# Kernel optimization log

Hardware: AMD Instinct MI355X
Metric: run time of the kernel (lower is better)

## Reference

```python
import jax, jax.numpy as jnp
import numpy as np

LOG2 = 0.6931471805599453
CUTOFF = 5.0
NG = 25

def ssp(x):
    # shifted softplus used throughout schnetpack
    return jax.nn.softplus(x) - LOG2

def setup_inputs() -> dict:
    key = jax.random.key(0)
    ks = jax.random.split(key, 10)
    B, A, N, F, Z, L = 8, 1024, 64, 128, 100, 3
    atomic_numbers = jax.random.randint(ks[0], (B, A), 0, Z, dtype=jnp.int32)
    positions = jax.random.normal(ks[1], (B, A, 3), dtype=jnp.float32) * 3.0
    cell = jnp.zeros((B, 3, 3), jnp.float32)
    cell_offset = jnp.zeros((B, A, N, 3), jnp.float32)
    neighbors = jax.random.randint(ks[2], (B, A, N), 0, A, dtype=jnp.int32)
    neighbor_mask = jnp.ones((B, A, N), jnp.float32)
    embed = (jax.random.normal(ks[3], (Z, F), dtype=jnp.float32) * 0.1).at[0].set(0.0)  # padding_idx=0
    p = lambda k, s: jax.random.normal(k, s, dtype=jnp.float32) * 0.1
    return dict(
        atomic_numbers=atomic_numbers, positions=positions, cell=cell,
        cell_offset=cell_offset, neighbors=neighbors, neighbor_mask=neighbor_mask,
        embed=embed,
        fw1=p(ks[4], (L, NG, F)), fb1=jnp.zeros((L, F), jnp.float32),
        fw2=p(ks[5], (L, F, F)), fb2=jnp.zeros((L, F), jnp.float32),
        in2f_w=p(ks[6], (L, F, F)),
        f2out_w=p(ks[7], (L, F, F)), f2out_b=jnp.zeros((L, F), jnp.float32),
        dense_w=p(ks[8], (L, F, F)), dense_b=jnp.zeros((L, F), jnp.float32),
    )

def reference(atomic_numbers, positions, cell, cell_offset, neighbors, neighbor_mask,
              embed, fw1, fb1, fw2, fb2, in2f_w, f2out_w, f2out_b, dense_w, dense_b):
    gather = jax.vmap(lambda a, i: a[i])  # per-batch neighbor gather
    x = embed[atomic_numbers]                                   # (B,A,F)
    # AtomDistances
    pos_j = gather(positions, neighbors)                        # (B,A,N,3)
    off = jnp.einsum('bani,bij->banj', cell_offset, cell)
    vec = pos_j - positions[:, :, None, :] + off
    d2 = jnp.sum(vec * vec, axis=-1)                            # (B,A,N)
    mask = neighbor_mask
    r = jnp.sqrt(jnp.where(mask > 0, d2, 1.0)) * mask           # masked distances
    # GaussianSmearing(0, cutoff, NG)
    goff = jnp.linspace(0.0, CUTOFF, NG)
    width = goff[1] - goff[0]
    f_ij = jnp.exp((-0.5 / (width * width)) * (r[..., None] - goff) ** 2)  # (B,A,N,NG)
    # CosineCutoff
    C = 0.5 * (jnp.cos(r * jnp.pi / CUTOFF) + 1.0) * (r < CUTOFF)
    for l in range(fw1.shape[0]):
        # filter-generating network (Dense+ssp, Dense)
        W = ssp(f_ij @ fw1[l] + fb1[l]) @ fw2[l] + fb2[l]       # (B,A,N,F)
        W = W * C[..., None]
        # CFConv: in2f (no bias) -> gather -> multiply -> masked sum -> f2out(ssp)
        y = x @ in2f_w[l]                                       # (B,A,F)
        y = gather(y, neighbors) * W * mask[..., None]          # (B,A,N,F)
        agg = jnp.sum(y, axis=2)                                # (B,A,F)
        v = ssp(agg @ f2out_w[l] + f2out_b[l])
        v = v @ dense_w[l] + dense_b[l]                         # interaction output dense
        x = x + v
    return x
```

## Files before the change

kernel.cpp:

```cpp
#include <hip/hip_runtime.h>
#include <hip/hip_fp16.h>
#include <math.h>

#define BB 8
#define AA 1024
#define NN 64
#define FF 128
#define NG 25

#define WIDTH 0.2083333333f
#define COEF  (-0.5f/(WIDTH*WIDTH))
#define PI_F  3.14159265358979f
#define CUTOFF 5.0f

#define KT 2048
#define HT (CUTOFF/(KT-1))
#define INVH ((float)(KT-1)/CUTOFF)

#define STR 132

typedef __attribute__((ext_vector_type(8))) short bf16x8;
typedef __attribute__((ext_vector_type(4))) short bf16x4;
typedef __attribute__((ext_vector_type(4))) float f32x4;

__device__ __forceinline__ float sspf(float x){
    return fmaxf(x, 0.f) + log1pf(expf(-fabsf(x))) - 0.69314718056f;
}
__device__ __forceinline__ short bf16r(float x){
    union { float f; unsigned u; } v; v.f = x;
    unsigned r = v.u + 0x7FFF + ((v.u >> 16) & 1);
    return (short)(r >> 16);
}
__device__ __forceinline__ __half2 h2bc(unsigned u){
    union { unsigned u; __half2 h; } v; v.u = u; return v.h;
}

__global__ __launch_bounds__(512) void k_prep(const float* __restrict__ pos,
                        const float* __restrict__ cell,
                        const float* __restrict__ coff, const int* __restrict__ nbr,
                        const float* __restrict__ mask,
                        const int* __restrict__ z, const float* __restrict__ emb,
                        const float* __restrict__ fw1, const float* __restrict__ fb1,
                        const float* __restrict__ fw2, const float* __restrict__ fb2,
                        const float* __restrict__ in2f, const float* __restrict__ f2w,
                        const float* __restrict__ dw,
                        unsigned* __restrict__ codes, int* __restrict__ cnt,
                        short* __restrict__ Wp,
                        __half* __restrict__ T, float* __restrict__ x,
                        __half* __restrict__ y){
    __shared__ __align__(16) char smem[NG*FF*4 + 16*28*4 + 16*STR*2];
    float* s_w1 = (float*)smem;
    float* s_g  = (float*)(smem + NG*FF*4);
    short* s_a  = (short*)(smem + NG*FF*4 + 16*28*4);
    __shared__ int s_cnt[16];

    int p = blockIdx.x;
    int tid = threadIdx.x, wv = tid >> 6, lane = tid & 63;
    int m = lane & 15, q = lane >> 4;
    int col = 16*wv + m;

    if(p < 512){
        int row0 = ((p & 7)*64 + (p >> 3))*16;
        if(tid < 16) s_cnt[tid] = 0;
        __syncthreads();
        #pragma unroll
        for(int u = 0; u < 2; u++){
            int pr = 2*tid + u;
            int rr = pr >> 6, n = pr & 63;
            int row = row0 + rr;
            int b = row >> 10;
            int flat = row*NN + n;
            int j = nbr[flat];
            const float* pi = pos + (size_t)row*3;
            const float* pj = pos + (size_t)(b*AA + j)*3;
            const float* co = coff + (size_t)flat*3;
            const float* cl = cell + b*9;
            float ox = co[0]*cl[0] + co[1]*cl[3] + co[2]*cl[6];
            float oy = co[0]*cl[1] + co[1]*cl[4] + co[2]*cl[7];
            float oz = co[0]*cl[2] + co[1]*cl[5] + co[2]*cl[8];
            float vx = pj[0]-pi[0]+ox, vy = pj[1]-pi[1]+oy, vz = pj[2]-pi[2]+oz;
            float d2 = vx*vx + vy*vy + vz*vz;
            float mk = mask[flat];
            float r  = sqrtf(mk > 0.f ? d2 : 1.0f) * mk;
            if(mk > 0.f && r < CUTOFF){
                int iv = (int)(r*INVH + 0.5f);
                if(iv > KT-1) iv = KT-1;
                int pos_ = atomicAdd(&s_cnt[rr], 1);
                codes[row*NN + pos_] = (unsigned)iv | ((unsigned)j << 16);
            }
        }
        __syncthreads();
        if(tid < 16){
            int c = s_cnt[tid];
            cnt[row0 + tid] = c;
            int cp = (c + 3) & ~3;
            for(int k2 = c; k2 < cp; k2++)
                codes[(row0 + tid)*NN + k2] = (unsigned)(KT-1);
        }
        bf16x8 wf[4];
        #pragma unroll
        for(int ks = 0; ks < 4; ks++)
            #pragma unroll
            for(int i = 0; i < 8; i++)
                wf[ks][i] = bf16r(in2f[(32*ks + 8*q + i)*FF + col]);
        for(int i = tid; i < 16*FF; i += 512){
            int rr = i >> 7, f = i & (FF-1);
            float v = emb[z[row0+rr]*FF + f];
            x[(row0+rr)*FF + f] = v;
            s_a[rr*STR + f] = bf16r(v);
        }
        __syncthreads();
        f32x4 acc = {0.f,0.f,0.f,0.f};
        #pragma unroll
        for(int ks = 0; ks < 4; ks++){
            const short* ap = s_a + m*STR + 32*ks + 8*q;
            bf16x4 lo = *(const bf16x4*)ap;
            bf16x4 hi = *(const bf16x4*)(ap + 4);
            bf16x8 af;
            af[0]=lo[0]; af[1]=lo[1]; af[2]=lo[2]; af[3]=lo[3];
            af[4]=hi[0]; af[5]=hi[1]; af[6]=hi[2]; af[7]=hi[3];
            acc = __builtin_amdgcn_mfma_f32_16x16x32_bf16(af, wf[ks], acc, 0, 0, 0);
        }
        #pragma unroll
        for(int j = 0; j < 4; j++)
            y[(row0 + 4*q + j)*FF + col] = __float2half(acc[j]);
    } else if(p < 896){
        int tb = p - 512;
        int l = tb >> 7;
        int kb = tb & 127;
        const float* w2s = fw2 + l*16384;
        bf16x8 wf[4];
        #pragma unroll
        for(int ks = 0; ks < 4; ks++)
            #pragma unroll
            for(int i = 0; i < 8; i++)
                wf[ks][i] = bf16r(w2s[(32*ks + 8*q + i)*FF + col]);

        for(int i = tid; i < NG*FF; i += 512) s_w1[i] = fw1[l*NG*FF + i];
        for(int i = tid; i < 16*NG; i += 512){
            int kn = i/25, g = i - 25*kn;
            float d = (16*kb + kn)*HT - g*WIDTH;
            s_g[kn*28 + g] = expf(COEF*d*d);
        }
        __syncthreads();
        {
            int f = tid & (FF-1), g4 = tid >> 7;
            float b1v = fb1[l*FF + f];
            #pragma unroll
            for(int i = 0; i < 4; i++){
                int kn = g4 + 4*i;
                float zz = b1v;
                for(int g = 0; g < NG; g++)
                    zz = fmaf(s_g[kn*28 + g], s_w1[g*FF + f], zz);
                s_a[kn*STR + f] = bf16r(sspf(zz));
            }
        }
        __syncthreads();
        float b2 = fb2[l*FF + col];
        f32x4 acc = {b2, b2, b2, b2};
        #pragma unroll
        for(int ks = 0; ks < 4; ks++){
            const short* ap = s_a + m*STR + 32*ks + 8*q;
            bf16x4 lo = *(const bf16x4*)ap;
            bf16x4 hi = *(const bf16x4*)(ap + 4);
            bf16x8 af;
            af[0]=lo[0]; af[1]=lo[1]; af[2]=lo[2]; af[3]=lo[3];
            af[4]=hi[0]; af[5]=hi[1]; af[6]=hi[2]; af[7]=hi[3];
            acc = __builtin_amdgcn_mfma_f32_16x16x32_bf16(af, wf[ks], acc, 0, 0, 0);
        }
        #pragma unroll
        for(int j = 0; j < 4; j++){
            int kn = 16*kb + 4*q + j;
            float r = kn*HT;
            float C = (r < CUTOFF) ? 0.5f*(cosf(r*(PI_F/CUTOFF)) + 1.0f) : 0.f;
            T[(l*KT + kn)*FF + col] = __float2half(acc[j]*C);
        }
    } else {
        int idx = (p - 896)*512 + tid;
        int id = idx >> 14, rem = idx & 16383;
        int ks = rem >> 12, nt = (rem >> 9) & 7, ln = (rem >> 3) & 63, i = rem & 7;
        int k = 32*ks + 8*(ln >> 4) + i;
        int f = 16*nt + (ln & 15);
        const float* src = (id < 3) ? f2w + id*16384
                         : (id < 6) ? dw  + (id-3)*16384
                                    : in2f + (id-5)*16384;
        Wp[idx] = bf16r(src[k*FF + f]);
    }
}

__global__ __launch_bounds__(512) void k_layerM(const unsigned* __restrict__ codes,
                                                const int* __restrict__ cnt,
                                                const __half* __restrict__ Tl,
                                                const __half* __restrict__ yin,
                                                const short* __restrict__ w1p,
                                                const float* __restrict__ f2b,
                                                const short* __restrict__ w2p,
                                                const float* __restrict__ db,
                                                const short* __restrict__ w3p,
                                                float* __restrict__ x,
                                                __half* __restrict__ ynext){
    __shared__ unsigned s_code[16*NN];
    __shared__ short s_a[16*STR];
    __shared__ short s_t[16*STR];

    int tid = threadIdx.x, wv = tid >> 6, lane = tid & 63;
    int m = lane & 15, q = lane >> 4;
    int p = blockIdx.x;
    int b = p & 7;
    int row0 = (b*64 + (p >> 3))*16;
    int col = 16*wv + m;

    float bias1 = f2b[col], bias2 = db[col];
    float xr[4];
    #pragma unroll
    for(int j = 0; j < 4; j++) xr[j] = x[(row0 + 4*q + j)*FF + col];

    *(uint2*)&s_code[2*tid] = *(const uint2*)&codes[row0*NN + 2*tid];
    __syncthreads();

    int qf = lane >> 4, fl = lane & 15, f8 = 8*fl;
    const __half* yb = yin + ((size_t)b*AA << 7) + f8;
    const __half* tb = Tl + f8;
    int a0 = 2*wv, a1 = 2*wv + 1;
    int n0 = (cnt[row0 + a0] + 3) >> 2;
    int n1 = (cnt[row0 + a1] + 3) >> 2;
    int nmax = n0 > n1 ? n0 : n1;
    __half2 hz = __float2half2_rn(0.f);
    __half2 pa[4] = {hz,hz,hz,hz}, pb[4] = {hz,hz,hz,hz};
    float ca[8] = {0,0,0,0,0,0,0,0}, cb[8] = {0,0,0,0,0,0,0,0};
    #pragma unroll 2
    for(int t = 0; t < nmax; t++){
        if(t < n0){
            unsigned cda = s_code[a0*NN + 4*t + qf];
            uint4 tva = *(const uint4*)(tb + ((cda & 0xFFFFu) << 7));
            uint4 yva = *(const uint4*)(yb + ((size_t)(cda >> 16) << 7));
            pa[0] = __hfma2(h2bc(tva.x), h2bc(yva.x), pa[0]);
            pa[1] = __hfma2(h2bc(tva.y), h2bc(yva.y), pa[1]);
            pa[2] = __hfma2(h2bc(tva.z), h2bc(yva.z), pa[2]);
            pa[3] = __hfma2(h2bc(tva.w), h2bc(yva.w), pa[3]);
        }
        if(t < n1){
            unsigned cdb = s_code[a1*NN + 4*t + qf];
            uint4 tvb = *(const uint4*)(tb + ((cdb & 0xFFFFu) << 7));
            uint4 yvb = *(const uint4*)(yb + ((size_t)(cdb >> 16) << 7));
            pb[0] = __hfma2(h2bc(tvb.x), h2bc(yvb.x), pb[0]);
            pb[1] = __hfma2(h2bc(tvb.y), h2bc(yvb.y), pb[1]);
            pb[2] = __hfma2(h2bc(tvb.z), h2bc(yvb.z), pb[2]);
            pb[3] = __hfma2(h2bc(tvb.w), h2bc(yvb.w), pb[3]);
        }
        if((t & 3) == 3){
            #pragma unroll
            for(int c2 = 0; c2 < 4; c2++){
                float2 ua = __half22float2(pa[c2]);
                float2 ub = __half22float2(pb[c2]);
                ca[2*c2]   += ua.x; ca[2*c2+1] += ua.y;
                cb[2*c2]   += ub.x; cb[2*c2+1] += ub.y;
                pa[c2] = hz; pb[c2] = hz;
            }
        }
    }
    #pragma unroll
    for(int c2 = 0; c2 < 4; c2++){
        float2 ua = __half22float2(pa[c2]);
        float2 ub = __half22float2(pb[c2]);
        ca[2*c2]   += ua.x; ca[2*c2+1] += ua.y;
        cb[2*c2]   += ub.x; cb[2*c2+1] += ub.y;
    }
    #pragma unroll
    for(int i = 0; i < 8; i++){
        ca[i] += __shfl_xor(ca[i], 16);
        ca[i] += __shfl_xor(ca[i], 32);
        cb[i] += __shfl_xor(cb[i], 16);
        cb[i] += __shfl_xor(cb[i], 32);
    }
    if(qf == 0){
        unsigned w0 = (unsigned short)bf16r(ca[0]) | ((unsigned)(unsigned short)bf16r(ca[1]) << 16);
        unsigned w1 = (unsigned short)bf16r(ca[2]) | ((unsigned)(unsigned short)bf16r(ca[3]) << 16);
        unsigned w2 = (unsigned short)bf16r(ca[4]) | ((unsigned)(unsigned short)bf16r(ca[5]) << 16);
        unsigned w3 = (unsigned short)bf16r(ca[6]) | ((unsigned)(unsigned short)bf16r(ca[7]) << 16);
        uint2 u01 = {w0, w1}, u23 = {w2, w3};
        *(uint2*)&s_a[a0*STR + f8]     = u01;
        *(uint2*)&s_a[a0*STR + f8 + 4] = u23;
        unsigned v0 = (unsigned short)bf16r(cb[0]) | ((unsigned)(unsigned short)bf16r(cb[1]) << 16);
        unsigned v1 = (unsigned short)bf16r(cb[2]) | ((unsigned)(unsigned short)bf16r(cb[3]) << 16);
        unsigned v2 = (unsigned short)bf16r(cb[4]) | ((unsigned)(unsigned short)bf16r(cb[5]) << 16);
        unsigned v3 = (unsigned short)bf16r(cb[6]) | ((unsigned)(unsigned short)bf16r(cb[7]) << 16);
        uint2 s01 = {v0, v1}, s23 = {v2, v3};
        *(uint2*)&s_a[a1*STR + f8]     = s01;
        *(uint2*)&s_a[a1*STR + f8 + 4] = s23;
    }

    unsigned long long w1o = (unsigned long long)w1p;
    asm volatile("" : "+s"(w1o));
    bf16x8 wfa[4];
    {
        const bf16x8* w1v = (const bf16x8*)w1o;
        #pragma unroll
        for(int ks = 0; ks < 4; ks++) wfa[ks] = w1v[(ks*8 + wv)*64 + lane];
    }
    __syncthreads();

    f32x4 acc = {bias1, bias1, bias1, bias1};
    #pragma unroll
    for(int ks = 0; ks < 4; ks++){
        const short* ap = s_a + m*STR + 32*ks + 8*q;
        bf16x4 lo = *(const bf16x4*)ap;
        bf16x4 hi = *(const bf16x4*)(ap + 4);
        bf16x8 af;
        af[0]=lo[0]; af[1]=lo[1]; af[2]=lo[2]; af[3]=lo[3];
        af[4]=hi[0]; af[5]=hi[1]; af[6]=hi[2]; af[7]=hi[3];
        acc = __builtin_amdgcn_mfma_f32_16x16x32_bf16(af, wfa[ks], acc, 0, 0, 0);
    }

    unsigned long long w2o = (unsigned long long)w2p;
    asm volatile("" : "+s"(w2o));
    bf16x8 wfb[4];
    {
        const bf16x8* w2v = (const bf16x8*)w2o;
        #pragma unroll
        for(int ks = 0; ks < 4; ks++) wfb[ks] = w2v[(ks*8 + wv)*64 + lane];
    }

    #pragma unroll
    for(int j = 0; j < 4; j++)
        s_t[(4*q + j)*STR + col] = bf16r(sspf(acc[j]));
    __syncthreads();

    f32x4 a2 = {bias2, bias2, bias2, bias2};
    #pragma unroll
    for(int ks = 0; ks < 4; ks++){
        const short* ap = s_t + m*STR + 32*ks + 8*q;
        bf16x4 lo = *(const bf16x4*)ap;
        bf16x4 hi = *(const bf16x4*)(ap + 4);
        bf16x8 af;
        af[0]=lo[0]; af[1]=lo[1]; af[2]=lo[2]; af[3]=lo[3];
        af[4]=hi[0]; af[5]=hi[1]; af[6]=hi[2]; af[7]=hi[3];
        a2 = __builtin_amdgcn_mfma_f32_16x16x32_bf16(af, wfb[ks], a2, 0, 0, 0);
    }

    float xn[4];
    #pragma unroll
    for(int j = 0; j < 4; j++){
        xn[j] = xr[j] + a2[j];
        x[(row0 + 4*q + j)*FF + col] = xn[j];
    }
    if(w3p){
        unsigned long long w3o = (unsigned long long)w3p;
        asm volatile("" : "+s"(w3o));
        bf16x8 wfc[4];
        {
            const bf16x8* w3v = (const bf16x8*)w3o;
            #pragma unroll
            for(int ks = 0; ks < 4; ks++) wfc[ks] = w3v[(ks*8 + wv)*64 + lane];
        }
        #pragma unroll
        for(int j = 0; j < 4; j++)
            s_a[(4*q + j)*STR + col] = bf16r(xn[j]);
        __syncthreads();
        f32x4 a3 = {0.f, 0.f, 0.f, 0.f};
        #pragma unroll
        for(int ks = 0; ks < 4; ks++){
            const short* ap = s_a + m*STR + 32*ks + 8*q;
            bf16x4 lo = *(const bf16x4*)ap;
            bf16x4 hi = *(const bf16x4*)(ap + 4);
            bf16x8 af;
            af[0]=lo[0]; af[1]=lo[1]; af[2]=lo[2]; af[3]=lo[3];
            af[4]=hi[0]; af[5]=hi[1]; af[6]=hi[2]; af[7]=hi[3];
            a3 = __builtin_amdgcn_mfma_f32_16x16x32_bf16(af, wfc[ks], a3, 0, 0, 0);
        }
        #pragma unroll
        for(int j = 0; j < 4; j++)
            ynext[(row0 + 4*q + j)*FF + col] = __float2half(a3[j]);
    }
}

extern "C" void kernel_launch(void* const* d_in, const int* in_sizes, int n_in,
                              void* d_out, int out_size, void* d_ws, size_t ws_size,
                              hipStream_t stream) {
    const int*   zat  = (const int*)  d_in[0];
    const float* pos  = (const float*)d_in[1];
    const float* cell = (const float*)d_in[2];
    const float* coff = (const float*)d_in[3];
    const int*   nbr  = (const int*)  d_in[4];
    const float* mask = (const float*)d_in[5];
    const float* emb  = (const float*)d_in[6];
    const float* fw1  = (const float*)d_in[7];
    const float* fb1  = (const float*)d_in[8];
    const float* fw2  = (const float*)d_in[9];
    const float* fb2  = (const float*)d_in[10];
    const float* in2f = (const float*)d_in[11];
    const float* f2w  = (const float*)d_in[12];
    const float* f2b  = (const float*)d_in[13];
    const float* dw   = (const float*)d_in[14];
    const float* db   = (const float*)d_in[15];

    float* x = (float*)d_out;
    unsigned* codes = (unsigned*)d_ws;
    __half* Tb = (__half*)(codes + BB*AA*NN);
    __half* yA = Tb + 3*KT*FF;
    __half* yB = yA + BB*AA*FF;
    short*  Wp = (short*)(yB + BB*AA*FF);
    int*    cnt = (int*)(Wp + 8*16384);

    k_prep<<<1152, 512, 0, stream>>>(pos, cell, coff, nbr, mask, zat, emb,
                                     fw1, fb1, fw2, fb2, in2f, f2w, dw,
                                     codes, cnt, Wp, Tb, x, yA);

    k_layerM<<<BB*AA/16, 512, 0, stream>>>(codes, cnt, Tb,           yA,
                                           Wp + 0*16384, f2b,        Wp + 3*16384, db,
                                           Wp + 6*16384, x, yB);
    k_layerM<<<BB*AA/16, 512, 0, stream>>>(codes, cnt, Tb + KT*FF,   yB,
                                           Wp + 1*16384, f2b + FF,   Wp + 4*16384, db + FF,
                                           Wp + 7*16384, x, yA);
    k_layerM<<<BB*AA/16, 512, 0, stream>>>(codes, cnt, Tb + 2*KT*FF, yA,
                                           Wp + 2*16384, f2b + 2*FF, Wp + 5*16384, db + 2*FF,
                                           nullptr, x, nullptr);
}
```

Before: 59.17 us.

## Fuse prep and three layer kernels into one cooperative persistent kernel

Replaces the four kernel launches (prep plus three layer kernels) with a single cooperative kernel of 512 blocks that uses grid-wide syncs between phases. Each block keeps its neighbor codes in shared memory and its x rows in registers across layers, so the global codes, counts and x round trips go away. Launch gaps are removed in exchange for grid barriers, and the whole grid must be co-resident, which depends on the occupancy check. If that check or the cooperative launch fails, the old multi-kernel path runs instead.

```diff
diff --git a/kernel.cpp b/kernel.cpp
--- a/kernel.cpp
+++ b/kernel.cpp
@@ -1,6 +1,9 @@
 #include <hip/hip_runtime.h>
 #include <hip/hip_fp16.h>
+#include <hip/hip_cooperative_groups.h>
 #include <math.h>
+
+namespace cg = cooperative_groups;
 
 #define BB 8
 #define AA 1024
@@ -33,6 +36,333 @@
 }
 __device__ __forceinline__ __half2 h2bc(unsigned u){
     union { unsigned u; __half2 h; } v; v.u = u; return v.h;
+}
+
+__global__ __launch_bounds__(512, 4) void k_all(const float* __restrict__ pos,
+                        const float* __restrict__ cell,
+                        const float* __restrict__ coff, const int* __restrict__ nbr,
+                        const float* __restrict__ mask,
+                        const int* __restrict__ z, const float* __restrict__ emb,
+                        const float* __restrict__ fw1, const float* __restrict__ fb1,
+                        const float* __restrict__ fw2, const float* __restrict__ fb2,
+                        const float* __restrict__ in2f, const float* __restrict__ f2w,
+                        const float* __restrict__ f2b, const float* __restrict__ dw,
+                        const float* __restrict__ db,
+                        short* __restrict__ Wp, __half* __restrict__ T,
+                        float* __restrict__ x, __half* __restrict__ yA,
+                        __half* __restrict__ yB){
+    __shared__ unsigned s_code[16*NN];
+    __shared__ int s_cnt[16];
+    __shared__ __align__(16) char smem[NG*FF*4 + 16*28*4 + 16*STR*2];
+
+    int p = blockIdx.x;
+    int tid = threadIdx.x, wv = tid >> 6, lane = tid & 63;
+    int m = lane & 15, q = lane >> 4;
+    int col = 16*wv + m;
+    int row0 = ((p & 7)*64 + (p >> 3))*16;
+    int b = row0 >> 10;
+
+    float* s_w1 = (float*)smem;
+    float* s_g  = (float*)(smem + NG*FF*4);
+    short* s_pa = (short*)(smem + NG*FF*4 + 16*28*4);
+
+    if(tid < 16) s_cnt[tid] = 0;
+    __syncthreads();
+    #pragma unroll
+    for(int u = 0; u < 2; u++){
+        int pr = 2*tid + u;
+        int rr = pr >> 6, n = pr & 63;
+        int row = row0 + rr;
+        int flat = row*NN + n;
+        int j = nbr[flat];
+        const float* pi = pos + (size_t)row*3;
+        const float* pj = pos + (size_t)(b*AA + j)*3;
+        const float* co = coff + (size_t)flat*3;
+        const float* cl = cell + b*9;
+        float ox = co[0]*cl[0] + co[1]*cl[3] + co[2]*cl[6];
+        float oy = co[0]*cl[1] + co[1]*cl[4] + co[2]*cl[7];
+        float oz = co[0]*cl[2] + co[1]*cl[5] + co[2]*cl[8];
+        float vx = pj[0]-pi[0]+ox, vy = pj[1]-pi[1]+oy, vz = pj[2]-pi[2]+oz;
+        float d2 = vx*vx + vy*vy + vz*vz;
+        float mk = mask[flat];
+        float r  = sqrtf(mk > 0.f ? d2 : 1.0f) * mk;
+        if(mk > 0.f && r < CUTOFF){
+            int iv = (int)(r*INVH + 0.5f);
+            if(iv > KT-1) iv = KT-1;
+            int ps = atomicAdd(&s_cnt[rr], 1);
+            s_code[rr*NN + ps] = (unsigned)iv | ((unsigned)j << 16);
+        }
+    }
+    __syncthreads();
+    if(tid < 16){
+        int c = s_cnt[tid];
+        int cp = (c + 3) & ~3;
+        for(int k2 = c; k2 < cp; k2++)
+            s_code[tid*NN + k2] = (unsigned)(KT-1);
+    }
+
+    float xr[4];
+    #pragma unroll
+    for(int j = 0; j < 4; j++) xr[j] = emb[z[row0 + 4*q + j]*FF + col];
+    for(int i = tid; i < 16*FF; i += 512){
+        int rr = i >> 7, f = i & (FF-1);
+        s_pa[rr*STR + f] = bf16r(emb[z[row0+rr]*FF + f]);
+    }
+    bf16x8 wf0[4];
+    #pragma unroll
+    for(int ks = 0; ks < 4; ks++)
+        #pragma unroll
+        for(int i = 0; i < 8; i++)
+            wf0[ks][i] = bf16r(in2f[(32*ks + 8*q + i)*FF + col]);
+    __syncthreads();
+    {
+        f32x4 acc = {0.f,0.f,0.f,0.f};
+        #pragma unroll
+        for(int ks = 0; ks < 4; ks++){
+            const short* ap = s_pa + m*STR + 32*ks + 8*q;
+            bf16x4 lo = *(const bf16x4*)ap;
+            bf16x4 hi = *(const bf16x4*)(ap + 4);
+            bf16x8 af;
+            af[0]=lo[0]; af[1]=lo[1]; af[2]=lo[2]; af[3]=lo[3];
+            af[4]=hi[0]; af[5]=hi[1]; af[6]=hi[2]; af[7]=hi[3];
+            acc = __builtin_amdgcn_mfma_f32_16x16x32_bf16(af, wf0[ks], acc, 0, 0, 0);
+        }
+        #pragma unroll
+        for(int j = 0; j < 4; j++)
+            yA[(row0 + 4*q + j)*FF + col] = __float2half(acc[j]);
+    }
+
+    if(p < 384){
+        __syncthreads();
+        int l = p >> 7, kb = p & 127;
+        const float* w2s = fw2 + l*16384;
+        bf16x8 wf[4];
+        #pragma unroll
+        for(int ks = 0; ks < 4; ks++)
+            #pragma unroll
+            for(int i = 0; i < 8; i++)
+                wf[ks][i] = bf16r(w2s[(32*ks + 8*q + i)*FF + col]);
+        for(int i = tid; i < NG*FF; i += 512) s_w1[i] = fw1[l*NG*FF + i];
+        for(int i = tid; i < 16*NG; i += 512){
+            int kn = i/25, g = i - 25*kn;
+            float d = (16*kb + kn)*HT - g*WIDTH;
+            s_g[kn*28 + g] = expf(COEF*d*d);
+        }
+        __syncthreads();
+        {
+            int f = tid & (FF-1), g4 = tid >> 7;
+            float b1v = fb1[l*FF + f];
+            #pragma unroll
+            for(int i = 0; i < 4; i++){
+                int kn = g4 + 4*i;
+                float zz = b1v;
+                for(int g = 0; g < NG; g++)
+                    zz = fmaf(s_g[kn*28 + g], s_w1[g*FF + f], zz);
+                s_pa[kn*STR + f] = bf16r(sspf(zz));
+            }
+        }
+        __syncthreads();
+        float b2 = fb2[l*FF + col];
+        f32x4 acc = {b2, b2, b2, b2};
+        #pragma unroll
+        for(int ks = 0; ks < 4; ks++){
+            const short* ap = s_pa + m*STR + 32*ks + 8*q;
+            bf16x4 lo = *(const bf16x4*)ap;
+            bf16x4 hi = *(const bf16x4*)(ap + 4);
+            bf16x8 af;
+            af[0]=lo[0]; af[1]=lo[1]; af[2]=lo[2]; af[3]=lo[3];
+            af[4]=hi[0]; af[5]=hi[1]; af[6]=hi[2]; af[7]=hi[3];
+            acc = __builtin_amdgcn_mfma_f32_16x16x32_bf16(af, wf[ks], acc, 0, 0, 0);
+        }
+        #pragma unroll
+        for(int j = 0; j < 4; j++){
+            int kn = 16*kb + 4*q + j;
+            float r = kn*HT;
+            float C = (r < CUTOFF) ? 0.5f*(cosf(r*(PI_F/CUTOFF)) + 1.0f) : 0.f;
+            T[(l*KT + kn)*FF + col] = __float2half(acc[j]*C);
+        }
+    } else {
+        int base = (p - 384)*1024;
+        #pragma unroll
+        for(int e = 0; e < 2; e++){
+            int idx = base + e*512 + tid;
+            int id = idx >> 14, rem = idx & 16383;
+            int ks = rem >> 12, nt = (rem >> 9) & 7, ln = (rem >> 3) & 63, i = rem & 7;
+            int k = 32*ks + 8*(ln >> 4) + i;
+            int f = 16*nt + (ln & 15);
+            const float* src = (id < 3) ? f2w + id*16384
+                             : (id < 6) ? dw  + (id-3)*16384
+                                        : in2f + (id-5)*16384;
+            Wp[idx] = bf16r(src[k*FF + f]);
+        }
+    }
+
+    cg::this_grid().sync();
+
+    short* s_a = (short*)smem;
+    short* s_t = (short*)(smem + 16*STR*2);
+    int qf = lane >> 4, fl = lane & 15, f8 = 8*fl;
+    int a0 = 2*wv, a1 = 2*wv + 1;
+    int n0 = (s_cnt[a0] + 3) >> 2;
+    int n1 = (s_cnt[a1] + 3) >> 2;
+    int nmax = n0 > n1 ? n0 : n1;
+
+    for(int l = 0; l < 3; l++){
+        const __half* yin  = (l == 1) ? yB : yA;
+        __half*       yout = (l == 0) ? yB : yA;
+        const __half* tb = T + (size_t)l*KT*FF + f8;
+        const __half* yb = yin + ((size_t)b*AA << 7) + f8;
+        float bias1 = f2b[l*FF + col], bias2 = db[l*FF + col];
+
+        __half2 hz = __float2half2_rn(0.f);
+        __half2 pa[4] = {hz,hz,hz,hz}, pb[4] = {hz,hz,hz,hz};
+        float ca[8] = {0,0,0,0,0,0,0,0}, cb[8] = {0,0,0,0,0,0,0,0};
+        #pragma unroll 2
+        for(int t = 0; t < nmax; t++){
+            if(t < n0){
+                unsigned cda = s_code[a0*NN + 4*t + qf];
+                uint4 tva = *(const uint4*)(tb + ((cda & 0xFFFFu) << 7));
+                uint4 yva = *(const uint4*)(yb + ((size_t)(cda >> 16) << 7));
+                pa[0] = __hfma2(h2bc(tva.x), h2bc(yva.x), pa[0]);
+                pa[1] = __hfma2(h2bc(tva.y), h2bc(yva.y), pa[1]);
+                pa[2] = __hfma2(h2bc(tva.z), h2bc(yva.z), pa[2]);
+                pa[3] = __hfma2(h2bc(tva.w), h2bc(yva.w), pa[3]);
+            }
+            if(t < n1){
+                unsigned cdb = s_code[a1*NN + 4*t + qf];
+                uint4 tvb = *(const uint4*)(tb + ((cdb & 0xFFFFu) << 7));
+                uint4 yvb = *(const uint4*)(yb + ((size_t)(cdb >> 16) << 7));
+                pb[0] = __hfma2(h2bc(tvb.x), h2bc(yvb.x), pb[0]);
+                pb[1] = __hfma2(h2bc(tvb.y), h2bc(yvb.y), pb[1]);
+                pb[2] = __hfma2(h2bc(tvb.z), h2bc(yvb.z), pb[2]);
+                pb[3] = __hfma2(h2bc(tvb.w), h2bc(yvb.w), pb[3]);
+            }
+            if((t & 3) == 3){
+                #pragma unroll
+                for(int c2 = 0; c2 < 4; c2++){
+                    float2 ua = __half22float2(pa[c2]);
+                    float2 ub = __half22float2(pb[c2]);
+                    ca[2*c2]   += ua.x; ca[2*c2+1] += ua.y;
+                    cb[2*c2]   += ub.x; cb[2*c2+1] += ub.y;
+                    pa[c2] = hz; pb[c2] = hz;
+                }
+            }
+        }
+        #pragma unroll
+        for(int c2 = 0; c2 < 4; c2++){
+            float2 ua = __half22float2(pa[c2]);
+            float2 ub = __half22float2(pb[c2]);
+            ca[2*c2]   += ua.x; ca[2*c2+1] += ua.y;
+            cb[2*c2]   += ub.x; cb[2*c2+1] += ub.y;
+        }
+        #pragma unroll
+        for(int i = 0; i < 8; i++){
+            ca[i] += __shfl_xor(ca[i], 16);
+            ca[i] += __shfl_xor(ca[i], 32);
+            cb[i] += __shfl_xor(cb[i], 16);
+            cb[i] += __shfl_xor(cb[i], 32);
+        }
+        if(qf == 0){
+            unsigned w0 = (unsigned short)bf16r(ca[0]) | ((unsigned)(unsigned short)bf16r(ca[1]) << 16);
+            unsigned w1 = (unsigned short)bf16r(ca[2]) | ((unsigned)(unsigned short)bf16r(ca[3]) << 16);
+            unsigned w2 = (unsigned short)bf16r(ca[4]) | ((unsigned)(unsigned short)bf16r(ca[5]) << 16);
+            unsigned w3 = (unsigned short)bf16r(ca[6]) | ((unsigned)(unsigned short)bf16r(ca[7]) << 16);
+            uint2 u01 = {w0, w1}, u23 = {w2, w3};
+            *(uint2*)&s_a[a0*STR + f8]     = u01;
+            *(uint2*)&s_a[a0*STR + f8 + 4] = u23;
+            unsigned v0 = (unsigned short)bf16r(cb[0]) | ((unsigned)(unsigned short)bf16r(cb[1]) << 16);
+            unsigned v1 = (unsigned short)bf16r(cb[2]) | ((unsigned)(unsigned short)bf16r(cb[3]) << 16);
+            unsigned v2 = (unsigned short)bf16r(cb[4]) | ((unsigned)(unsigned short)bf16r(cb[5]) << 16);
+            unsigned v3 = (unsigned short)bf16r(cb[6]) | ((unsigned)(unsigned short)bf16r(cb[7]) << 16);
+            uint2 s01 = {v0, v1}, s23 = {v2, v3};
+            *(uint2*)&s_a[a1*STR + f8]     = s01;
+            *(uint2*)&s_a[a1*STR + f8 + 4] = s23;
+        }
+
+        unsigned long long w1o = (unsigned long long)(Wp + l*16384);
+        asm volatile("" : "+s"(w1o));
+        bf16x8 wfa[4];
+        {
+            const bf16x8* w1v = (const bf16x8*)w1o;
+            #pragma unroll
+            for(int ks = 0; ks < 4; ks++) wfa[ks] = w1v[(ks*8 + wv)*64 + lane];
+        }
+        __syncthreads();
+
+        f32x4 acc = {bias1, bias1, bias1, bias1};
+        #pragma unroll
+        for(int ks = 0; ks < 4; ks++){
+            const short* ap = s_a + m*STR + 32*ks + 8*q;
+            bf16x4 lo = *(const bf16x4*)ap;
+            bf16x4 hi = *(const bf16x4*)(ap + 4);
+            bf16x8 af;
+            af[0]=lo[0]; af[1]=lo[1]; af[2]=lo[2]; af[3]=lo[3];
+            af[4]=hi[0]; af[5]=hi[1]; af[6]=hi[2]; af[7]=hi[3];
+            acc = __builtin_amdgcn_mfma_f32_16x16x32_bf16(af, wfa[ks], acc, 0, 0, 0);
+        }
+
+        unsigned long long w2o = (unsigned long long)(Wp + (3 + l)*16384);
+        asm volatile("" : "+s"(w2o));
+        bf16x8 wfb[4];
+        {
+            const bf16x8* w2v = (const bf16x8*)w2o;
+            #pragma unroll
+            for(int ks = 0; ks < 4; ks++) wfb[ks] = w2v[(ks*8 + wv)*64 + lane];
+        }
+
+        #pragma unroll
+        for(int j = 0; j < 4; j++)
+            s_t[(4*q + j)*STR + col] = bf16r(sspf(acc[j]));
+        __syncthreads();
+
+        f32x4 a2 = {bias2, bias2, bias2, bias2};
+        #pragma unroll
+        for(int ks = 0; ks < 4; ks++){
+            const short* ap = s_t + m*STR + 32*ks + 8*q;
+            bf16x4 lo = *(const bf16x4*)ap;
+            bf16x4 hi = *(const bf16x4*)(ap + 4);
+            bf16x8 af;
+            af[0]=lo[0]; af[1]=lo[1]; af[2]=lo[2]; af[3]=lo[3];
+            af[4]=hi[0]; af[5]=hi[1]; af[6]=hi[2]; af[7]=hi[3];
+            a2 = __builtin_amdgcn_mfma_f32_16x16x32_bf16(af, wfb[ks], a2, 0, 0, 0);
+        }
+        #pragma unroll
+        for(int j = 0; j < 4; j++) xr[j] += a2[j];
+
+        if(l < 2){
+            unsigned long long w3o = (unsigned long long)(Wp + (6 + l)*16384);
+            asm volatile("" : "+s"(w3o));
+            bf16x8 wfc[4];
+            {
+                const bf16x8* w3v = (const bf16x8*)w3o;
+                #pragma unroll
+                for(int ks = 0; ks < 4; ks++) wfc[ks] = w3v[(ks*8 + wv)*64 + lane];
+            }
+            #pragma unroll
+            for(int j = 0; j < 4; j++)
+                s_a[(4*q + j)*STR + col] = bf16r(xr[j]);
+            __syncthreads();
+            f32x4 a3 = {0.f, 0.f, 0.f, 0.f};
+            #pragma unroll
+            for(int ks = 0; ks < 4; ks++){
+                const short* ap = s_a + m*STR + 32*ks + 8*q;
+                bf16x4 lo = *(const bf16x4*)ap;
+                bf16x4 hi = *(const bf16x4*)(ap + 4);
+                bf16x8 af;
+                af[0]=lo[0]; af[1]=lo[1]; af[2]=lo[2]; af[3]=lo[3];
+                af[4]=hi[0]; af[5]=hi[1]; af[6]=hi[2]; af[7]=hi[3];
+                a3 = __builtin_amdgcn_mfma_f32_16x16x32_bf16(af, wfc[ks], a3, 0, 0, 0);
+            }
+            #pragma unroll
+            for(int j = 0; j < 4; j++)
+                yout[(row0 + 4*q + j)*FF + col] = __float2half(a3[j]);
+            cg::this_grid().sync();
+        }
+    }
+
+    #pragma unroll
+    for(int j = 0; j < 4; j++)
+        x[(row0 + 4*q + j)*FF + col] = xr[j];
 }
 
 __global__ __launch_bounds__(512) void k_prep(const float* __restrict__ pos,
@@ -135,7 +465,6 @@
             #pragma unroll
             for(int i = 0; i < 8; i++)
                 wf[ks][i] = bf16r(w2s[(32*ks + 8*q + i)*FF + col]);
-
         for(int i = tid; i < NG*FF; i += 512) s_w1[i] = fw1[l*NG*FF + i];
         for(int i = tid; i < 16*NG; i += 512){
             int kn = i/25, g = i - 25*kn;
@@ -402,17 +731,31 @@
     short*  Wp = (short*)(yB + BB*AA*FF);
     int*    cnt = (int*)(Wp + 8*16384);
 
-    k_prep<<<1152, 512, 0, stream>>>(pos, cell, coff, nbr, mask, zat, emb,
-                                     fw1, fb1, fw2, fb2, in2f, f2w, dw,
-                                     codes, cnt, Wp, Tb, x, yA);
-
-    k_layerM<<<BB*AA/16, 512, 0, stream>>>(codes, cnt, Tb,           yA,
-                                           Wp + 0*16384, f2b,        Wp + 3*16384, db,
-                                           Wp + 6*16384, x, yB);
-    k_layerM<<<BB*AA/16, 512, 0, stream>>>(codes, cnt, Tb + KT*FF,   yB,
-                                           Wp + 1*16384, f2b + FF,   Wp + 4*16384, db + FF,
-                                           Wp + 7*16384, x, yA);
-    k_layerM<<<BB*AA/16, 512, 0, stream>>>(codes, cnt, Tb + 2*KT*FF, yA,
-                                           Wp + 2*16384, f2b + 2*FF, Wp + 5*16384, db + 2*FF,
-                                           nullptr, x, nullptr);
+    int nb = 0;
+    hipError_t qe = hipOccupancyMaxActiveBlocksPerMultiprocessor(&nb, k_all, 512, 0);
+    bool coop = (qe == hipSuccess && nb >= 2);
+    if(coop){
+        void* args[] = {(void*)&pos, (void*)&cell, (void*)&coff, (void*)&nbr,
+                        (void*)&mask, (void*)&zat, (void*)&emb, (void*)&fw1,
+                        (void*)&fb1, (void*)&fw2, (void*)&fb2, (void*)&in2f,
+                        (void*)&f2w, (void*)&f2b, (void*)&dw, (void*)&db,
+                        (void*)&Wp, (void*)&Tb, (void*)&x, (void*)&yA, (void*)&yB};
+        hipError_t le = hipLaunchCooperativeKernel(k_all, dim3(512), dim3(512),
+                                                   args, 0u, stream);
+        if(le != hipSuccess) coop = false;
+    }
+    if(!coop){
+        k_prep<<<1152, 512, 0, stream>>>(pos, cell, coff, nbr, mask, zat, emb,
+                                         fw1, fb1, fw2, fb2, in2f, f2w, dw,
+                                         codes, cnt, Wp, Tb, x, yA);
+        k_layerM<<<BB*AA/16, 512, 0, stream>>>(codes, cnt, Tb,           yA,
+                                               Wp + 0*16384, f2b,        Wp + 3*16384, db,
+                                               Wp + 6*16384, x, yB);
+        k_layerM<<<BB*AA/16, 512, 0, stream>>>(codes, cnt, Tb + KT*FF,   yB,
+                                               Wp + 1*16384, f2b + FF,   Wp + 4*16384, db + FF,
+                                               Wp + 7*16384, x, yA);
+        k_layerM<<<BB*AA/16, 512, 0, stream>>>(codes, cnt, Tb + 2*KT*FF, yA,
+                                               Wp + 2*16384, f2b + 2*FF, Wp + 5*16384, db + 2*FF,
+                                               nullptr, x, nullptr);
+    }
 }
```

After: 59.43 us. About the same (+0.4%).

## Halve filter table, stage neighbor codes in LDS, drop per-iteration gather predicates

Applied to the files above, without the earlier changes.

Halves the distance lookup table from 2048 to 1024 entries, which cuts the filter-network table-building blocks in the prep kernel. Neighbor codes are now compacted in shared memory, pre-filled with a sentinel, and written to global memory with one coalesced vector store. The gather loop no longer checks each atom's own count; it processes both atoms up to the larger count and relies on sentinel entries that point at a zero table row, with deeper unrolling. The x residual load moves after the aggregation. The coarser table raises interpolation error in the filter values, and atoms with fewer neighbors now do some wasted gathers.

```diff
diff --git a/kernel.cpp b/kernel.cpp
--- a/kernel.cpp
+++ b/kernel.cpp
@@ -13,9 +13,10 @@
 #define PI_F  3.14159265358979f
 #define CUTOFF 5.0f
 
-#define KT 2048
+#define KT 1024
 #define HT (CUTOFF/(KT-1))
 #define INVH ((float)(KT-1)/CUTOFF)
+#define SENT ((unsigned)(KT-1))
 
 #define STR 132
 
@@ -52,6 +53,7 @@
     float* s_w1 = (float*)smem;
     float* s_g  = (float*)(smem + NG*FF*4);
     short* s_a  = (short*)(smem + NG*FF*4 + 16*28*4);
+    __shared__ unsigned s_codeP[16*NN];
     __shared__ int s_cnt[16];
 
     int p = blockIdx.x;
@@ -62,6 +64,8 @@
     if(p < 512){
         int row0 = ((p & 7)*64 + (p >> 3))*16;
         if(tid < 16) s_cnt[tid] = 0;
+        s_codeP[2*tid]   = SENT;
+        s_codeP[2*tid+1] = SENT;
         __syncthreads();
         #pragma unroll
         for(int u = 0; u < 2; u++){
@@ -85,18 +89,14 @@
             if(mk > 0.f && r < CUTOFF){
                 int iv = (int)(r*INVH + 0.5f);
                 if(iv > KT-1) iv = KT-1;
-                int pos_ = atomicAdd(&s_cnt[rr], 1);
-                codes[row*NN + pos_] = (unsigned)iv | ((unsigned)j << 16);
+                int ps = atomicAdd(&s_cnt[rr], 1);
+                s_codeP[rr*NN + ps] = (unsigned)iv | ((unsigned)j << 16);
             }
         }
         __syncthreads();
-        if(tid < 16){
-            int c = s_cnt[tid];
-            cnt[row0 + tid] = c;
-            int cp = (c + 3) & ~3;
-            for(int k2 = c; k2 < cp; k2++)
-                codes[(row0 + tid)*NN + k2] = (unsigned)(KT-1);
-        }
+        *(uint2*)&codes[row0*NN + 2*tid] = *(uint2*)&s_codeP[2*tid];
+        if(tid < 16) cnt[row0 + tid] = s_cnt[tid];
+
         bf16x8 wf[4];
         #pragma unroll
         for(int ks = 0; ks < 4; ks++)
@@ -124,10 +124,10 @@
         #pragma unroll
         for(int j = 0; j < 4; j++)
             y[(row0 + 4*q + j)*FF + col] = __float2half(acc[j]);
-    } else if(p < 896){
+    } else if(p < 704){
         int tb = p - 512;
-        int l = tb >> 7;
-        int kb = tb & 127;
+        int l = tb >> 6;
+        int kb = tb & 63;
         const float* w2s = fw2 + l*16384;
         bf16x8 wf[4];
         #pragma unroll
@@ -176,7 +176,7 @@
             T[(l*KT + kn)*FF + col] = __float2half(acc[j]*C);
         }
     } else {
-        int idx = (p - 896)*512 + tid;
+        int idx = (p - 704)*512 + tid;
         int id = idx >> 14, rem = idx & 16383;
         int ks = rem >> 12, nt = (rem >> 9) & 7, ln = (rem >> 3) & 63, i = rem & 7;
         int k = 32*ks + 8*(ln >> 4) + i;
@@ -211,9 +211,6 @@
     int col = 16*wv + m;
 
     float bias1 = f2b[col], bias2 = db[col];
-    float xr[4];
-    #pragma unroll
-    for(int j = 0; j < 4; j++) xr[j] = x[(row0 + 4*q + j)*FF + col];
 
     *(uint2*)&s_code[2*tid] = *(const uint2*)&codes[row0*NN + 2*tid];
     __syncthreads();
@@ -222,32 +219,28 @@
     const __half* yb = yin + ((size_t)b*AA << 7) + f8;
     const __half* tb = Tl + f8;
     int a0 = 2*wv, a1 = 2*wv + 1;
-    int n0 = (cnt[row0 + a0] + 3) >> 2;
-    int n1 = (cnt[row0 + a1] + 3) >> 2;
-    int nmax = n0 > n1 ? n0 : n1;
+    int c0 = cnt[row0 + a0], c1 = cnt[row0 + a1];
+    int cm = c0 > c1 ? c0 : c1;
+    int nmax = (cm + 3) >> 2;
     __half2 hz = __float2half2_rn(0.f);
     __half2 pa[4] = {hz,hz,hz,hz}, pb[4] = {hz,hz,hz,hz};
     float ca[8] = {0,0,0,0,0,0,0,0}, cb[8] = {0,0,0,0,0,0,0,0};
-    #pragma unroll 2
+    #pragma unroll 4
     for(int t = 0; t < nmax; t++){
-        if(t < n0){
-            unsigned cda = s_code[a0*NN + 4*t + qf];
-            uint4 tva = *(const uint4*)(tb + ((cda & 0xFFFFu) << 7));
-            uint4 yva = *(const uint4*)(yb + ((size_t)(cda >> 16) << 7));
-            pa[0] = __hfma2(h2bc(tva.x), h2bc(yva.x), pa[0]);
-            pa[1] = __hfma2(h2bc(tva.y), h2bc(yva.y), pa[1]);
-            pa[2] = __hfma2(h2bc(tva.z), h2bc(yva.z), pa[2]);
-            pa[3] = __hfma2(h2bc(tva.w), h2bc(yva.w), pa[3]);
-        }
-        if(t < n1){
-            unsigned cdb = s_code[a1*NN + 4*t + qf];
-            uint4 tvb = *(const uint4*)(tb + ((cdb & 0xFFFFu) << 7));
-            uint4 yvb = *(const uint4*)(yb + ((size_t)(cdb >> 16) << 7));
-            pb[0] = __hfma2(h2bc(tvb.x), h2bc(yvb.x), pb[0]);
-            pb[1] = __hfma2(h2bc(tvb.y), h2bc(yvb.y), pb[1]);
-            pb[2] = __hfma2(h2bc(tvb.z), h2bc(yvb.z), pb[2]);
-            pb[3] = __hfma2(h2bc(tvb.w), h2bc(yvb.w), pb[3]);
-        }
+        unsigned cda = s_code[a0*NN + 4*t + qf];
+        unsigned cdb = s_code[a1*NN + 4*t + qf];
+        uint4 tva = *(const uint4*)(tb + ((cda & 0xFFFFu) << 7));
+        uint4 yva = *(const uint4*)(yb + ((size_t)(cda >> 16) << 7));
+        uint4 tvb = *(const uint4*)(tb + ((cdb & 0xFFFFu) << 7));
+        uint4 yvb = *(const uint4*)(yb + ((size_t)(cdb >> 16) << 7));
+        pa[0] = __hfma2(h2bc(tva.x), h2bc(yva.x), pa[0]);
+        pa[1] = __hfma2(h2bc(tva.y), h2bc(yva.y), pa[1]);
+        pa[2] = __hfma2(h2bc(tva.z), h2bc(yva.z), pa[2]);
+        pa[3] = __hfma2(h2bc(tva.w), h2bc(yva.w), pa[3]);
+        pb[0] = __hfma2(h2bc(tvb.x), h2bc(yvb.x), pb[0]);
+        pb[1] = __hfma2(h2bc(tvb.y), h2bc(yvb.y), pb[1]);
+        pb[2] = __hfma2(h2bc(tvb.z), h2bc(yvb.z), pb[2]);
+        pb[3] = __hfma2(h2bc(tvb.w), h2bc(yvb.w), pb[3]);
         if((t & 3) == 3){
             #pragma unroll
             for(int c2 = 0; c2 < 4; c2++){
@@ -288,6 +281,15 @@
         uint2 s01 = {v0, v1}, s23 = {v2, v3};
         *(uint2*)&s_a[a1*STR + f8]     = s01;
         *(uint2*)&s_a[a1*STR + f8 + 4] = s23;
+    }
+
+    unsigned long long xo = (unsigned long long)x;
+    asm volatile("" : "+s"(xo));
+    float xr[4];
+    {
+        const float* xro = (const float*)xo;
+        #pragma unroll
+        for(int j = 0; j < 4; j++) xr[j] = xro[(row0 + 4*q + j)*FF + col];
     }
 
     unsigned long long w1o = (unsigned long long)w1p;
@@ -402,9 +404,9 @@
     short*  Wp = (short*)(yB + BB*AA*FF);
     int*    cnt = (int*)(Wp + 8*16384);
 
-    k_prep<<<1152, 512, 0, stream>>>(pos, cell, coff, nbr, mask, zat, emb,
-                                     fw1, fb1, fw2, fb2, in2f, f2w, dw,
-                                     codes, cnt, Wp, Tb, x, yA);
+    k_prep<<<960, 512, 0, stream>>>(pos, cell, coff, nbr, mask, zat, emb,
+                                    fw1, fb1, fw2, fb2, in2f, f2w, dw,
+                                    codes, cnt, Wp, Tb, x, yA);
 
     k_layerM<<<BB*AA/16, 512, 0, stream>>>(codes, cnt, Tb,           yA,
                                            Wp + 0*16384, f2b,        Wp + 3*16384, db,
```

Result: faster. 52.15 us (-11.9%).
